# Kernel optimization log

Hardware: AMD Instinct MI355X
Metric: run time of the kernel (lower is better)

The kernel has to match this reference:

```python
import jax, jax.numpy as jnp
import numpy as np

B, O, S, C, H, W = 8, 8, 32, 64, 32, 32  # batch, N_out groups, spatial/sample, N_in channels, H, W
HID = C  # ratio = 1


def setup_inputs() -> dict:
    key = jax.random.key(0)
    k1, k2, k3 = jax.random.split(key, 3)
    x = jax.random.normal(k1, (B, O, S, C, H, W), dtype=jnp.float32)
    # kaiming_uniform_(a=sqrt(5)) -> U(-1/sqrt(fan_in), 1/sqrt(fan_in)), fan_in = last dim
    b1 = 1.0 / np.sqrt(C)
    b2 = 1.0 / np.sqrt(HID)
    w1 = jax.random.uniform(k2, (O, HID, C), minval=-b1, maxval=b1, dtype=jnp.float32)
    w2 = jax.random.uniform(k3, (O, C, HID), minval=-b2, maxval=b2, dtype=jnp.float32)
    return {"x": x, "w1": w1, "w2": w2}


def reference(x, w1, w2):
    # Pool over spatial dims (H, W): [B,O,S,C]
    p_mean = x.mean(axis=(-2, -1))
    p_max = x.max(axis=(-2, -1))

    def grouped_mlp(p):
        # per-group FC1 + relu + FC2: original _linear broadcast-mul+sum == grouped GEMM
        h = jax.nn.relu(jnp.einsum('bosc,ohc->bosh', p, w1))
        return jnp.einsum('bosh,onh->bosn', h, w2)

    out = jax.nn.sigmoid(grouped_mlp(p_mean) + grouped_mlp(p_max))
    # reshape to [B, N_out, S, N_in, 1, 1]
    return out[..., None, None]
```

## Files before the change

### kernel.cpp

```cpp
#include <hip/hip_runtime.h>
#include <math.h>

#define Bc 8
#define Oc 8
#define Sc 32
#define Cc 64
#define HWc 1024
#define NBLK (Bc*Oc*Sc)

__global__ __launch_bounds__(256) void ca_fused(const float* __restrict__ x,
                                                const float* __restrict__ w1,
                                                const float* __restrict__ w2,
                                                float* __restrict__ out) {
    __shared__ float s_mean[Cc];
    __shared__ float s_max[Cc];
    __shared__ float s_hm[Cc];
    __shared__ float s_hx[Cc];

    const int blk  = blockIdx.x;
    const int o    = (blk / Sc) % Oc;
    const int tid  = threadIdx.x;
    const int wave = tid >> 6;
    const int lane = tid & 63;

    const float* xb = x + (size_t)blk * (Cc * HWc);

    #pragma unroll 4
    for (int ci = 0; ci < 16; ++ci) {
        const int c = wave * 16 + ci;
        const float4* p = (const float4*)(xb + (size_t)c * HWc);
        float4 v0 = p[lane];
        float4 v1 = p[lane + 64];
        float4 v2 = p[lane + 128];
        float4 v3 = p[lane + 192];

        float sum = (v0.x + v0.y) + (v0.z + v0.w)
                  + (v1.x + v1.y) + (v1.z + v1.w)
                  + (v2.x + v2.y) + (v2.z + v2.w)
                  + (v3.x + v3.y) + (v3.z + v3.w);
        float mx  = fmaxf(fmaxf(fmaxf(v0.x, v0.y), fmaxf(v0.z, v0.w)),
                    fmaxf(fmaxf(fmaxf(v1.x, v1.y), fmaxf(v1.z, v1.w)),
                    fmaxf(fmaxf(fmaxf(v2.x, v2.y), fmaxf(v2.z, v2.w)),
                          fmaxf(fmaxf(v3.x, v3.y), fmaxf(v3.z, v3.w)))));

        #pragma unroll
        for (int m = 32; m >= 1; m >>= 1) {
            sum += __shfl_xor(sum, m, 64);
            mx   = fmaxf(mx, __shfl_xor(mx, m, 64));
        }
        if (lane == 0) {
            s_mean[c] = sum * (1.0f / 1024.0f);
            s_max[c]  = mx;
        }
    }
    __syncthreads();

    if (tid < Cc) {
        const float* w1o = w1 + ((size_t)o * Cc + tid) * Cc;
        float am = 0.f, ax = 0.f;
        #pragma unroll
        for (int c2 = 0; c2 < Cc; ++c2) {
            const float w = w1o[c2];
            am = fmaf(s_mean[c2], w, am);
            ax = fmaf(s_max[c2],  w, ax);
        }
        s_hm[tid] = fmaxf(am, 0.f);
        s_hx[tid] = fmaxf(ax, 0.f);
    }
    __syncthreads();

    if (tid < Cc) {
        const float* w2o = w2 + ((size_t)o * Cc + tid) * Cc;
        float am = 0.f, ax = 0.f;
        #pragma unroll
        for (int h = 0; h < Cc; ++h) {
            const float w = w2o[h];
            am = fmaf(s_hm[h], w, am);
            ax = fmaf(s_hx[h], w, ax);
        }
        const float z = am + ax;
        out[(size_t)blk * Cc + tid] = 1.0f / (1.0f + __expf(-z));
    }
}

extern "C" void kernel_launch(void* const* d_in, const int* in_sizes, int n_in,
                              void* d_out, int out_size, void* d_ws, size_t ws_size,
                              hipStream_t stream) {
    const float* x  = (const float*)d_in[0];
    const float* w1 = (const float*)d_in[1];
    const float* w2 = (const float*)d_in[2];
    float* out = (float*)d_out;

    ca_fused<<<NBLK, 256, 0, stream>>>(x, w1, w2, out);
}
```

Baseline: 673.1 us.

## Use nontemporal loads, two channels per iteration, and split MLP across two waves

The pooling loop now processes two channels per iteration, issuing eight nontemporal vector loads at once and interleaving two shuffle reductions, so more memory requests are in flight. The mean and max MLP paths are split across two waves instead of one wave doing both, which halves the serial FMA chain per thread. This costs an extra shared array and an extra barrier. The nontemporal hint is meant to keep streaming x data from polluting the cache.

```diff
diff --git a/kernel.cpp b/kernel.cpp
--- a/kernel.cpp
+++ b/kernel.cpp
@@ -8,6 +8,15 @@
 #define HWc 1024
 #define NBLK (Bc*Oc*Sc)
 
+typedef float f4 __attribute__((ext_vector_type(4)));
+
+static __device__ __forceinline__ float hsum(f4 a) { return (a.x + a.y) + (a.z + a.w); }
+static __device__ __forceinline__ float hmax(f4 a) { return fmaxf(fmaxf(a.x, a.y), fmaxf(a.z, a.w)); }
+static __device__ __forceinline__ f4 vmax4(f4 a, f4 b) {
+    f4 r; r.x = fmaxf(a.x, b.x); r.y = fmaxf(a.y, b.y);
+    r.z = fmaxf(a.z, b.z); r.w = fmaxf(a.w, b.w); return r;
+}
+
 __global__ __launch_bounds__(256) void ca_fused(const float* __restrict__ x,
                                                 const float* __restrict__ w1,
                                                 const float* __restrict__ w2,
@@ -16,6 +25,7 @@
     __shared__ float s_max[Cc];
     __shared__ float s_hm[Cc];
     __shared__ float s_hx[Cc];
+    __shared__ float s_ax[Cc];
 
     const int blk  = blockIdx.x;
     const int o    = (blk / Sc) % Oc;
@@ -23,63 +33,70 @@
     const int wave = tid >> 6;
     const int lane = tid & 63;
 
-    const float* xb = x + (size_t)blk * (Cc * HWc);
+    const f4* xb = (const f4*)(x + (size_t)blk * (Cc * HWc)) + lane;
 
-    #pragma unroll 4
-    for (int ci = 0; ci < 16; ++ci) {
-        const int c = wave * 16 + ci;
-        const float4* p = (const float4*)(xb + (size_t)c * HWc);
-        float4 v0 = p[lane];
-        float4 v1 = p[lane + 64];
-        float4 v2 = p[lane + 128];
-        float4 v3 = p[lane + 192];
+    #pragma unroll
+    for (int g = 0; g < 8; ++g) {
+        const int c0 = wave * 16 + g * 2;
+        const f4* p0 = xb + (size_t)c0 * 256;
+        const f4* p1 = p0 + 256;
 
-        float sum = (v0.x + v0.y) + (v0.z + v0.w)
-                  + (v1.x + v1.y) + (v1.z + v1.w)
-                  + (v2.x + v2.y) + (v2.z + v2.w)
-                  + (v3.x + v3.y) + (v3.z + v3.w);
-        float mx  = fmaxf(fmaxf(fmaxf(v0.x, v0.y), fmaxf(v0.z, v0.w)),
-                    fmaxf(fmaxf(fmaxf(v1.x, v1.y), fmaxf(v1.z, v1.w)),
-                    fmaxf(fmaxf(fmaxf(v2.x, v2.y), fmaxf(v2.z, v2.w)),
-                          fmaxf(fmaxf(v3.x, v3.y), fmaxf(v3.z, v3.w)))));
+        f4 a0 = __builtin_nontemporal_load(p0);
+        f4 a1 = __builtin_nontemporal_load(p0 + 64);
+        f4 a2 = __builtin_nontemporal_load(p0 + 128);
+        f4 a3 = __builtin_nontemporal_load(p0 + 192);
+        f4 b0 = __builtin_nontemporal_load(p1);
+        f4 b1 = __builtin_nontemporal_load(p1 + 64);
+        f4 b2 = __builtin_nontemporal_load(p1 + 128);
+        f4 b3 = __builtin_nontemporal_load(p1 + 192);
+
+        f4 sa = (a0 + a1) + (a2 + a3);
+        f4 ma = vmax4(vmax4(a0, a1), vmax4(a2, a3));
+        f4 sb = (b0 + b1) + (b2 + b3);
+        f4 mb = vmax4(vmax4(b0, b1), vmax4(b2, b3));
+
+        float s0 = hsum(sa), m0 = hmax(ma);
+        float s1 = hsum(sb), m1 = hmax(mb);
 
         #pragma unroll
         for (int m = 32; m >= 1; m >>= 1) {
-            sum += __shfl_xor(sum, m, 64);
-            mx   = fmaxf(mx, __shfl_xor(mx, m, 64));
+            s0 += __shfl_xor(s0, m, 64);
+            s1 += __shfl_xor(s1, m, 64);
+            m0 = fmaxf(m0, __shfl_xor(m0, m, 64));
+            m1 = fmaxf(m1, __shfl_xor(m1, m, 64));
         }
         if (lane == 0) {
-            s_mean[c] = sum * (1.0f / 1024.0f);
-            s_max[c]  = mx;
+            s_mean[c0]     = s0 * (1.0f / 1024.0f);
+            s_mean[c0 + 1] = s1 * (1.0f / 1024.0f);
+            s_max[c0]      = m0;
+            s_max[c0 + 1]  = m1;
         }
     }
     __syncthreads();
 
-    if (tid < Cc) {
-        const float* w1o = w1 + ((size_t)o * Cc + tid) * Cc;
-        float am = 0.f, ax = 0.f;
+    float acc2 = 0.f;
+    if (wave < 2) {
+        const float* src = wave ? s_max : s_mean;
+        const float* w1o = w1 + ((size_t)o * Cc + lane) * Cc;
+        float a = 0.f;
         #pragma unroll
-        for (int c2 = 0; c2 < Cc; ++c2) {
-            const float w = w1o[c2];
-            am = fmaf(s_mean[c2], w, am);
-            ax = fmaf(s_max[c2],  w, ax);
-        }
-        s_hm[tid] = fmaxf(am, 0.f);
-        s_hx[tid] = fmaxf(ax, 0.f);
+        for (int c2 = 0; c2 < Cc; ++c2) a = fmaf(src[c2], w1o[c2], a);
+        (wave ? s_hx : s_hm)[lane] = fmaxf(a, 0.f);
     }
     __syncthreads();
 
-    if (tid < Cc) {
-        const float* w2o = w2 + ((size_t)o * Cc + tid) * Cc;
-        float am = 0.f, ax = 0.f;
+    if (wave < 2) {
+        const float* src = wave ? s_hx : s_hm;
+        const float* w2o = w2 + ((size_t)o * Cc + lane) * Cc;
         #pragma unroll
-        for (int h = 0; h < Cc; ++h) {
-            const float w = w2o[h];
-            am = fmaf(s_hm[h], w, am);
-            ax = fmaf(s_hx[h], w, ax);
-        }
-        const float z = am + ax;
-        out[(size_t)blk * Cc + tid] = 1.0f / (1.0f + __expf(-z));
+        for (int h = 0; h < Cc; ++h) acc2 = fmaf(src[h], w2o[h], acc2);
+        if (wave == 1) s_ax[lane] = acc2;
+    }
+    __syncthreads();
+
+    if (wave == 0) {
+        const float z = acc2 + s_ax[lane];
+        out[(size_t)blk * Cc + lane] = 1.0f / (1.0f + __expf(-z));
     }
 }
 
```

New measurement: 649.5 us. 1.04x faster.
